# Performance work log

Measured on AMD Instinct MI355X. Metric: run time of the kernel, lower is better.

Reference implementation:

```python
import jax, jax.numpy as jnp
import numpy as np

H = 8      # num_attention_heads
DH = 96    # attention_head_size
LN_EPS = 1e-5


def setup_inputs() -> dict:
    key = jax.random.key(0)
    ks = jax.random.split(key, 12)
    B, S, D = 2, 768, 768
    sc = 0.02
    return {
        "hidden_states": jax.random.normal(ks[0], (B, S, D), jnp.float32),
        "distance_matrix": jax.random.uniform(ks[1], (B, S, S), jnp.float32) * 20.0,
        "angle_matrix": jax.random.uniform(ks[2], (B, S, S), jnp.float32) * np.pi,
        "attention_mask": jnp.ones((B, S), jnp.float32),
        "Wq": jax.random.normal(ks[3], (D, D), jnp.float32) * sc,
        "bq": jnp.zeros((D,), jnp.float32),
        "Wk": jax.random.normal(ks[4], (D, D), jnp.float32) * sc,
        "bk": jnp.zeros((D,), jnp.float32),
        "Wv": jax.random.normal(ks[5], (D, D), jnp.float32) * sc,
        "bv": jnp.zeros((D,), jnp.float32),
        "Wd": jax.random.normal(ks[6], (DH,), jnp.float32) * sc,
        "bd": jnp.zeros((DH,), jnp.float32),
        "Wa": jax.random.normal(ks[7], (DH,), jnp.float32) * sc,
        "ba": jnp.zeros((DH,), jnp.float32),
        "Wo": jax.random.normal(ks[8], (D, D), jnp.float32) * sc,
        "bo": jnp.zeros((D,), jnp.float32),
        "ln_g": jnp.ones((D,), jnp.float32),
        "ln_b": jnp.zeros((D,), jnp.float32),
    }


def _heads(x, B, S):
    # [B,S,D] -> [B,H,S,DH]
    return x.reshape(B, S, H, DH).transpose(0, 2, 1, 3)


def reference(hidden_states, distance_matrix, angle_matrix, attention_mask,
              Wq, bq, Wk, bk, Wv, bv, Wd, bd, Wa, ba, Wo, bo, ln_g, ln_b):
    B, S, D = hidden_states.shape
    q = _heads(hidden_states @ Wq.T + bq, B, S)   # [B,H,S,DH]
    k = _heads(hidden_states @ Wk.T + bk, B, S)
    v = _heads(hidden_states @ Wv.T + bv, B, S)

    scores = jnp.einsum('bhid,bhjd->bhij', q, k) / jnp.sqrt(jnp.float32(DH))

    # distance / angle relative-position biases: emb[b,i,j,:] = dist[b,i,j]*Wd + bd
    dist_emb = distance_matrix[..., None] * Wd + bd   # [B,S,S,DH]
    scores = scores + jnp.einsum('bhid,bijd->bhij', q, dist_emb)
    ang_emb = angle_matrix[..., None] * Wa + ba       # [B,S,S,DH]
    scores = scores + jnp.einsum('bhid,bijd->bhij', q, ang_emb)

    # key mask, broadcast over heads and query positions
    scores = scores + (1.0 - attention_mask)[:, None, None, :] * -10000.0

    probs = jax.nn.softmax(scores, axis=-1)           # [B,H,S,S]
    ctx = jnp.einsum('bhij,bhjd->bhid', probs, v)
    ctx = ctx.transpose(0, 2, 1, 3).reshape(B, S, D)  # [B,S,D]

    out = ctx @ Wo.T + bo
    x = out + hidden_states
    mu = jnp.mean(x, axis=-1, keepdims=True)
    var = jnp.var(x, axis=-1, keepdims=True)
    out = (x - mu) * jax.lax.rsqrt(var + LN_EPS) * ln_g + ln_b
    return out, probs
```

## Files before the change

### kernel.cpp

```cpp
#include <hip/hip_runtime.h>
#include <stdint.h>

#define B_  2
#define S_  768
#define D_  768
#define H_  8
#define DH_ 96

typedef unsigned short ushort_t;
typedef __bf16 bf16x8 __attribute__((ext_vector_type(8)));
typedef float  f32x4  __attribute__((ext_vector_type(4)));

__device__ inline ushort_t f2bf(float f) {
    union { float f; unsigned int u; } v; v.f = f;
    unsigned int u = v.u;
    unsigned int r = u + 0x7fffu + ((u >> 16) & 1u);
    return (ushort_t)(r >> 16);
}
__device__ inline float bf2f(ushort_t u) {
    union { unsigned int i; float f; } c; c.i = ((unsigned int)u) << 16;
    return c.f;
}

__device__ inline void glds16(const void* gp, void* lp) {
    auto g = reinterpret_cast<const __attribute__((address_space(1))) uint32_t*>(
        reinterpret_cast<uintptr_t>(gp));
    auto l = reinterpret_cast<__attribute__((address_space(3))) uint32_t*>(
        reinterpret_cast<uintptr_t>(lp));
    __builtin_amdgcn_global_load_lds(g, l, 16, 0, 0);
}

__global__ __launch_bounds__(256) void k_convert(
        const float* __restrict__ X, const float* __restrict__ Wq,
        const float* __restrict__ Wk, const float* __restrict__ Wv,
        const float* __restrict__ Wo,
        ushort_t* __restrict__ Xb, ushort_t* __restrict__ Wb) {
    const int NX4 = (B_ * S_ * D_) / 4;
    const int NW4 = (D_ * D_) / 4;
    int i = blockIdx.x * blockDim.x + threadIdx.x;
    float4 v;
    ushort_t* dst;
    if (i < NX4) {
        v = ((const float4*)X)[i];
        dst = Xb + i * 4;
    } else {
        int wi = i - NX4;
        int sel = wi / NW4;
        int off = wi - sel * NW4;
        const float* src = (sel == 0) ? Wq : (sel == 1) ? Wk : (sel == 2) ? Wv : Wo;
        v = ((const float4*)src)[off];
        dst = Wb + wi * 4;
    }
    ushort4 o;
    o.x = f2bf(v.x); o.y = f2bf(v.y); o.z = f2bf(v.z); o.w = f2bf(v.w);
    *(ushort4*)dst = o;
}

__device__ inline void gemm64_dbuf(
        const ushort_t* __restrict__ A, int lda,
        const ushort_t* __restrict__ Bt, int ldb,
        int K, int m0, int n0,
        ushort_t* As, ushort_t* Bs, f32x4 acc[2][2]) {
    const int tid  = threadIdx.x;
    const int lane = tid & 63, wave = tid >> 6;
    const int wm = (wave >> 1) * 32, wn = (wave & 1) * 32;
    const int fr = lane & 15, fk = (lane >> 4) * 8;
    const ushort_t* Ap = A  + (size_t)(m0 + wave * 16 + (lane >> 2)) * lda + (lane & 3) * 8;
    const ushort_t* Bp = Bt + (size_t)(n0 + wave * 16 + (lane >> 2)) * ldb + (lane & 3) * 8;
    glds16(Ap, As + wave * 512);
    glds16(Bp, Bs + wave * 512);
    for (int kt = 0; kt < K; kt += 32) {
        const int cur = (kt >> 5) & 1;
        __syncthreads();
        if (kt + 32 < K) {
            glds16(Ap + kt + 32, As + (cur ^ 1) * 2048 + wave * 512);
            glds16(Bp + kt + 32, Bs + (cur ^ 1) * 2048 + wave * 512);
        }
        const ushort_t* Ab = As + cur * 2048;
        const ushort_t* Bb = Bs + cur * 2048;
        bf16x8 a0 = *(const bf16x8*)&Ab[(wm      + fr) * 32 + fk];
        bf16x8 a1 = *(const bf16x8*)&Ab[(wm + 16 + fr) * 32 + fk];
        bf16x8 b0 = *(const bf16x8*)&Bb[(wn      + fr) * 32 + fk];
        bf16x8 b1 = *(const bf16x8*)&Bb[(wn + 16 + fr) * 32 + fk];
        acc[0][0] = __builtin_amdgcn_mfma_f32_16x16x32_bf16(a0, b0, acc[0][0], 0, 0, 0);
        acc[0][1] = __builtin_amdgcn_mfma_f32_16x16x32_bf16(a0, b1, acc[0][1], 0, 0, 0);
        acc[1][0] = __builtin_amdgcn_mfma_f32_16x16x32_bf16(a1, b0, acc[1][0], 0, 0, 0);
        acc[1][1] = __builtin_amdgcn_mfma_f32_16x16x32_bf16(a1, b1, acc[1][1], 0, 0, 0);
    }
}

__global__ __launch_bounds__(256) void k_qkv(
        const ushort_t* __restrict__ Xb, const ushort_t* __restrict__ Wb,
        const float* __restrict__ bq, const float* __restrict__ bk,
        const float* __restrict__ bv,
        ushort_t* __restrict__ Qb, ushort_t* __restrict__ Kb,
        ushort_t* __restrict__ Vtb) {
    __shared__ __align__(16) ushort_t As[2 * 64 * 32];
    __shared__ __align__(16) ushort_t Bs[2 * 64 * 32];
    f32x4 acc[2][2];
    #pragma unroll
    for (int i = 0; i < 2; i++)
        #pragma unroll
        for (int j = 0; j < 2; j++) acc[i][j] = (f32x4){0.f, 0.f, 0.f, 0.f};
    const int m0 = blockIdx.y * 64, n0 = blockIdx.x * 64;
    gemm64_dbuf(Xb, D_, Wb, D_, D_, m0, n0, As, Bs, acc);
    const int lane = threadIdx.x & 63, wave = threadIdx.x >> 6;
    const int wm = (wave >> 1) * 32, wn = (wave & 1) * 32;
    #pragma unroll
    for (int ni = 0; ni < 2; ni++) {
        int gcol = n0 + wn + ni * 16 + (lane & 15);
        int gsel = gcol / D_, d768 = gcol - gsel * D_;
        int h = d768 / DH_, d = d768 - h * DH_;
        float bias = (gsel == 0 ? bq : (gsel == 1 ? bk : bv))[d768];
        #pragma unroll
        for (int mi = 0; mi < 2; mi++) {
            int grow0 = m0 + wm + mi * 16 + (lane >> 4) * 4;
            int b = grow0 / S_, s0 = grow0 - b * S_;
            int bh = b * H_ + h;
            if (gsel == 2) {
                ushort4 o4;
                o4.x = f2bf(acc[mi][ni][0] + bias);
                o4.y = f2bf(acc[mi][ni][1] + bias);
                o4.z = f2bf(acc[mi][ni][2] + bias);
                o4.w = f2bf(acc[mi][ni][3] + bias);
                *(ushort4*)&Vtb[((size_t)bh * DH_ + d) * S_ + s0] = o4;
            } else {
                #pragma unroll
                for (int r = 0; r < 4; r++) {
                    ushort_t ob = f2bf(acc[mi][ni][r] + bias);
                    if (gsel == 0) Qb[((size_t)bh * S_ + s0 + r) * DH_ + d] = ob;
                    else           Kb[((size_t)bh * S_ + s0 + r) * DH_ + d] = ob;
                }
            }
        }
    }
}

__global__ __launch_bounds__(256) void k_qcoef(
        const ushort_t* __restrict__ Qb,
        const float* __restrict__ Wd, const float* __restrict__ bd,
        const float* __restrict__ Wa, const float* __restrict__ ba,
        float* __restrict__ qcoef) {
    const int wave = threadIdx.x >> 6, lane = threadIdx.x & 63;
    const int row = blockIdx.x * 4 + wave;
    const ushort_t* q = Qb + (size_t)row * DH_;
    float e0 = bf2f(q[lane]);
    float c0 = e0 * Wd[lane];
    float c1 = e0 * Wa[lane];
    float c2 = e0 * (bd[lane] + ba[lane]);
    if (lane < 32) {
        int d = 64 + lane;
        float e1 = bf2f(q[d]);
        c0 += e1 * Wd[d];
        c1 += e1 * Wa[d];
        c2 += e1 * (bd[d] + ba[d]);
    }
    #pragma unroll
    for (int o = 32; o > 0; o >>= 1) {
        c0 += __shfl_down(c0, o);
        c1 += __shfl_down(c1, o);
        c2 += __shfl_down(c2, o);
    }
    if (lane == 0) {
        qcoef[row * 3 + 0] = c0;
        qcoef[row * 3 + 1] = c1;
        qcoef[row * 3 + 2] = c2;
    }
}

#define FL1B 20480
__global__ __launch_bounds__(256, 3) void k_flash(
        const ushort_t* __restrict__ Qb, const ushort_t* __restrict__ Kb,
        const ushort_t* __restrict__ Vtb, const float* __restrict__ qcoef,
        const float* __restrict__ distm, const float* __restrict__ angm,
        const float* __restrict__ mask,
        float* __restrict__ probs, ushort_t* __restrict__ Ctxb) {
    __shared__ __align__(16) char sm[2 * FL1B + 512];
    float* mstat = (float*)(sm + 2 * FL1B);
    float* lstat = (float*)(sm + 2 * FL1B + 256);
    const int idx = blockIdx.x;
    const int h = idx / 96, rem = idx - h * 96;
    const int b = rem / 48, r0 = (rem - b * 48) * 16;
    const int bh = b * H_ + h;
    const int tid = threadIdx.x, lane = tid & 63, w = tid >> 6;
    const int frn = lane & 15, g = lane >> 4;
    const ushort_t* Qbh = Qb + (size_t)bh * S_ * DH_;
    const ushort_t* Kbh = Kb + (size_t)bh * S_ * DH_;
    const ushort_t* Vbh = Vtb + (size_t)bh * DH_ * S_;

    auto stage = [&](int c) {
        char* bufc = sm + (c & 1) * FL1B;
        ushort_t* Ks = (ushort_t*)bufc;
        const ushort_t* kg = Kbh + (size_t)c * 64 * DH_;
        #pragma unroll
        for (int t = 0; t < 3; ++t) {
            int grp = w * 3 + t;
            glds16(kg + (size_t)lane * DH_ + grp * 8, Ks + grp * 512);
        }
        int row = 4 * w + g;
        int colb = (frn ^ (row & 7)) << 2;
        size_t src = ((size_t)b * S_ + r0 + row) * S_ + c * 64 + colb;
        glds16(distm + src, (float*)(bufc + 12288) + w * 256);
        glds16(angm  + src, (float*)(bufc + 16384) + w * 256);
    };

    stage(0);

    bf16x8 aq0, aq1, aq2;
    {
        const ushort_t* qp = Qbh + (size_t)(r0 + frn) * DH_ + g * 8;
        aq0 = *(const bf16x8*)qp;
        aq1 = *(const bf16x8*)(qp + 32);
        aq2 = *(const bf16x8*)(qp + 64);
    }
    float qc0, qc1, qc2;
    {
        const float* qp = qcoef + ((size_t)bh * S_ + r0 + frn) * 3;
        qc0 = qp[0]; qc1 = qp[1]; qc2 = qp[2];
    }
    const float isq = 0.10206207261596577f;
    const int dswz = ((4 * w + g) ^ (frn & 7)) << 2;
    const int jrow = (16 * w + frn) * 8;

    f32x4 acc[12];
    __syncthreads();
    #pragma unroll
    for (int c = 0; c < 12; ++c) {
        if (c < 11) stage(c + 1);
        char* bufc = sm + (c & 1) * FL1B;
        const ushort_t* Ks = (const ushort_t*)bufc;
        const float* Dd = (const float*)(bufc + 12288);
        const float* Da = (const float*)(bufc + 16384);
        bf16x8 k0 = *(const bf16x8*)&Ks[(g    ) * 512 + jrow];
        bf16x8 k1 = *(const bf16x8*)&Ks[(g + 4) * 512 + jrow];
        bf16x8 k2 = *(const bf16x8*)&Ks[(g + 8) * 512 + jrow];
        f32x4 ca = (f32x4){0.f, 0.f, 0.f, 0.f};
        ca = __builtin_amdgcn_mfma_f32_16x16x32_bf16(k0, aq0, ca, 0, 0, 0);
        ca = __builtin_amdgcn_mfma_f32_16x16x32_bf16(k1, aq1, ca, 0, 0, 0);
        ca = __builtin_amdgcn_mfma_f32_16x16x32_bf16(k2, aq2, ca, 0, 0, 0);
        float4 d4 = *(const float4*)(Dd + frn * 64 + dswz);
        float4 a4 = *(const float4*)(Da + frn * 64 + dswz);
        float4 m4 = *(const float4*)(mask + b * S_ + c * 64 + w * 16 + g * 4);
        f32x4 o;
        o[0] = ca[0] * isq + d4.x * qc0 + a4.x * qc1 + qc2 + (1.f - m4.x) * -10000.f;
        o[1] = ca[1] * isq + d4.y * qc0 + a4.y * qc1 + qc2 + (1.f - m4.y) * -10000.f;
        o[2] = ca[2] * isq + d4.z * qc0 + a4.z * qc1 + qc2 + (1.f - m4.z) * -10000.f;
        o[3] = ca[3] * isq + d4.w * qc0 + a4.w * qc1 + qc2 + (1.f - m4.w) * -10000.f;
        acc[c] = o;
        __syncthreads();
    }

    float mx = -1e30f;
    #pragma unroll
    for (int c = 0; c < 12; ++c)
        #pragma unroll
        for (int r = 0; r < 4; ++r) mx = fmaxf(mx, acc[c][r]);
    mx = fmaxf(mx, __shfl_xor(mx, 16));
    mx = fmaxf(mx, __shfl_xor(mx, 32));
    if (g == 0) mstat[w * 16 + frn] = mx;
    __syncthreads();
    float mf = fmaxf(fmaxf(mstat[frn], mstat[16 + frn]),
                     fmaxf(mstat[32 + frn], mstat[48 + frn]));
    float sum = 0.f;
    #pragma unroll
    for (int c = 0; c < 12; ++c)
        #pragma unroll
        for (int r = 0; r < 4; ++r) {
            float e = __expf(acc[c][r] - mf);
            acc[c][r] = e;
            sum += e;
        }
    sum += __shfl_xor(sum, 16);
    sum += __shfl_xor(sum, 32);
    if (g == 0) lstat[w * 16 + frn] = sum;
    __syncthreads();
    float inv = 1.f / (lstat[frn] + lstat[16 + frn] + lstat[32 + frn] + lstat[48 + frn]);

    float* ctxred = (float*)sm;
    {
        int zr = tid >> 4, zc = tid & 15;
        #pragma unroll
        for (int i = 0; i < 6; ++i) ctxred[zr * 100 + i * 16 + zc] = 0.f;
    }
    __syncthreads();

    f32x4 accO[6];
    #pragma unroll
    for (int i = 0; i < 6; ++i) accO[i] = (f32x4){0.f, 0.f, 0.f, 0.f};
    float* prow = probs + ((size_t)bh * S_ + r0 + frn) * S_ + w * 16 + g * 4;
    const ushort_t* vbase = Vbh + (size_t)frn * S_ + w * 16 + g * 4;
    #pragma unroll
    for (int c = 0; c < 12; c += 2) {
        float4 p;
        p.x = acc[c][0] * inv; p.y = acc[c][1] * inv;
        p.z = acc[c][2] * inv; p.w = acc[c][3] * inv;
        *(float4*)(prow + c * 64) = p;
        p.x = acc[c + 1][0] * inv; p.y = acc[c + 1][1] * inv;
        p.z = acc[c + 1][2] * inv; p.w = acc[c + 1][3] * inv;
        *(float4*)(prow + (c + 1) * 64) = p;
        union { bf16x8 v; ushort_t u[8]; } pa;
        #pragma unroll
        for (int r = 0; r < 4; ++r) {
            pa.u[r]     = f2bf(acc[c][r]);
            pa.u[r + 4] = f2bf(acc[c + 1][r]);
        }
        #pragma unroll
        for (int nt = 0; nt < 6; ++nt) {
            const ushort_t* vp = vbase + (size_t)nt * 16 * S_ + c * 64;
            union { bf16x8 v; uint2 q2[2]; } vb;
            vb.q2[0] = *(const uint2*)vp;
            vb.q2[1] = *(const uint2*)(vp + 64);
            accO[nt] = __builtin_amdgcn_mfma_f32_16x16x32_bf16(pa.v, vb.v, accO[nt], 0, 0, 0);
        }
    }
    #pragma unroll
    for (int nt = 0; nt < 6; ++nt)
        #pragma unroll
        for (int r = 0; r < 4; ++r)
            atomicAdd(&ctxred[(4 * g + r) * 100 + nt * 16 + frn], accO[nt][r]);
    __syncthreads();
    {
        int zr = tid >> 4, zc = tid & 15;
        float ivr = 1.f / (lstat[zr] + lstat[16 + zr] + lstat[32 + zr] + lstat[48 + zr]);
        ushort_t* crow = Ctxb + ((size_t)b * S_ + r0 + zr) * D_ + h * DH_;
        #pragma unroll
        for (int i = 0; i < 6; ++i)
            crow[i * 16 + zc] = f2bf(ctxred[zr * 100 + i * 16 + zc] * ivr);
    }
}

__global__ __launch_bounds__(256) void k_out(
        const ushort_t* __restrict__ Ctxb, const ushort_t* __restrict__ Wob,
        const float* __restrict__ bo, const float* __restrict__ hidden,
        float* __restrict__ xbuf) {
    __shared__ __align__(16) ushort_t As[2 * 64 * 32];
    __shared__ __align__(16) ushort_t Bs[2 * 64 * 32];
    f32x4 acc[2][2];
    #pragma unroll
    for (int i = 0; i < 2; i++)
        #pragma unroll
        for (int j = 0; j < 2; j++) acc[i][j] = (f32x4){0.f, 0.f, 0.f, 0.f};
    const int m0 = blockIdx.y * 64, n0 = blockIdx.x * 64;
    gemm64_dbuf(Ctxb, D_, Wob, D_, D_, m0, n0, As, Bs, acc);
    const int lane = threadIdx.x & 63, wave = threadIdx.x >> 6;
    const int wm = (wave >> 1) * 32, wn = (wave & 1) * 32;
    #pragma unroll
    for (int ni = 0; ni < 2; ni++) {
        int gcol = n0 + wn + ni * 16 + (lane & 15);
        float bias = bo[gcol];
        #pragma unroll
        for (int mi = 0; mi < 2; mi++) {
            #pragma unroll
            for (int r = 0; r < 4; r++) {
                int grow = m0 + wm + mi * 16 + (lane >> 4) * 4 + r;
                xbuf[(size_t)grow * D_ + gcol] =
                    acc[mi][ni][r] + bias + hidden[(size_t)grow * D_ + gcol];
            }
        }
    }
}

__global__ __launch_bounds__(256) void k_ln(
        const float* __restrict__ xbuf, const float* __restrict__ g,
        const float* __restrict__ bb, float* __restrict__ out) {
    const float* x = xbuf + (size_t)blockIdx.x * D_;
    const int t = threadIdx.x;
    float a0 = x[t], a1 = x[t + 256], a2 = x[t + 512];
    float s = a0 + a1 + a2;
    float ss = a0 * a0 + a1 * a1 + a2 * a2;
    __shared__ float r1[4], r2[4];
    #pragma unroll
    for (int o = 32; o > 0; o >>= 1) { s += __shfl_down(s, o); ss += __shfl_down(ss, o); }
    if ((t & 63) == 0) { r1[t >> 6] = s; r2[t >> 6] = ss; }
    __syncthreads();
    float ts = r1[0] + r1[1] + r1[2] + r1[3];
    float tss = r2[0] + r2[1] + r2[2] + r2[3];
    float mu = ts * (1.0f / D_);
    float var = tss * (1.0f / D_) - mu * mu;
    float rstd = rsqrtf(var + 1e-5f);
    float* o = out + (size_t)blockIdx.x * D_;
    o[t]       = (a0 - mu) * rstd * g[t]       + bb[t];
    o[t + 256] = (a1 - mu) * rstd * g[t + 256] + bb[t + 256];
    o[t + 512] = (a2 - mu) * rstd * g[t + 512] + bb[t + 512];
}

extern "C" void kernel_launch(void* const* d_in, const int* in_sizes, int n_in,
                              void* d_out, int out_size, void* d_ws, size_t ws_size,
                              hipStream_t stream) {
    const float* X     = (const float*)d_in[0];
    const float* distm = (const float*)d_in[1];
    const float* angm  = (const float*)d_in[2];
    const float* mask  = (const float*)d_in[3];
    const float* Wq    = (const float*)d_in[4];
    const float* bq    = (const float*)d_in[5];
    const float* Wk    = (const float*)d_in[6];
    const float* bk    = (const float*)d_in[7];
    const float* Wv    = (const float*)d_in[8];
    const float* bv    = (const float*)d_in[9];
    const float* Wd    = (const float*)d_in[10];
    const float* bd    = (const float*)d_in[11];
    const float* Wa    = (const float*)d_in[12];
    const float* ba    = (const float*)d_in[13];
    const float* Wo    = (const float*)d_in[14];
    const float* bo    = (const float*)d_in[15];
    const float* ln_g  = (const float*)d_in[16];
    const float* ln_b  = (const float*)d_in[17];

    float* outp  = (float*)d_out;
    float* probs = (float*)d_out + (size_t)B_ * S_ * D_;

    char* ws = (char*)d_ws;
    ushort_t* Xb    = (ushort_t*)(ws + 0);
    ushort_t* Wb    = (ushort_t*)(ws + 2359296);
    ushort_t* Qb    = (ushort_t*)(ws + 7077888);
    ushort_t* Kb    = (ushort_t*)(ws + 9437184);
    ushort_t* Vtb   = (ushort_t*)(ws + 11796480);
    ushort_t* Ctxb  = (ushort_t*)(ws + 14155776);
    float*    qcoef = (float*)   (ws + 16515072);
    float*    xbuf  = (float*)   (ws + 16662528);

    k_convert<<<3456, 256, 0, stream>>>(X, Wq, Wk, Wv, Wo, Xb, Wb);
    k_qkv<<<dim3(36, 24), 256, 0, stream>>>(Xb, Wb, bq, bk, bv, Qb, Kb, Vtb);
    k_qcoef<<<3072, 256, 0, stream>>>(Qb, Wd, bd, Wa, ba, qcoef);
    k_flash<<<768, 256, 0, stream>>>(Qb, Kb, Vtb, qcoef, distm, angm, mask, probs, Ctxb);
    k_out<<<dim3(12, 24), 256, 0, stream>>>(Ctxb, Wb + (size_t)2304 * 768, bo, X, xbuf);
    k_ln<<<1536, 256, 0, stream>>>(xbuf, ln_g, ln_b, outp);
}
```

Measured before the change: 207.6 us.

## Stage V through double-buffered LDS and store K in chunked-d layout

K is now written by the QKV projection in a [bh][d/8][S][8] layout, so each 16-byte async global-to-LDS load in the flash kernel reads a contiguous span instead of striding by the head dimension. The PV phase no longer reads V directly from global memory with 8-byte loads. It async-copies 128-column V tiles into a double-buffered, XOR-swizzled LDS region, overlapping the next tile's load with the current MFMAs. This raises shared memory per block (2x24KB plus stats) and adds barriers per tile, which could reduce occupancy under the 3-blocks launch bound.

```diff
diff --git a/kernel.cpp b/kernel.cpp
--- a/kernel.cpp
+++ b/kernel.cpp
@@ -124,12 +124,17 @@
                 o4.z = f2bf(acc[mi][ni][2] + bias);
                 o4.w = f2bf(acc[mi][ni][3] + bias);
                 *(ushort4*)&Vtb[((size_t)bh * DH_ + d) * S_ + s0] = o4;
+            } else if (gsel == 1) {
+                #pragma unroll
+                for (int r = 0; r < 4; r++) {
+                    ushort_t ob = f2bf(acc[mi][ni][r] + bias);
+                    Kb[(((size_t)bh * 12 + (d >> 3)) * S_ + s0 + r) * 8 + (d & 7)] = ob;
+                }
             } else {
                 #pragma unroll
                 for (int r = 0; r < 4; r++) {
                     ushort_t ob = f2bf(acc[mi][ni][r] + bias);
-                    if (gsel == 0) Qb[((size_t)bh * S_ + s0 + r) * DH_ + d] = ob;
-                    else           Kb[((size_t)bh * S_ + s0 + r) * DH_ + d] = ob;
+                    Qb[((size_t)bh * S_ + s0 + r) * DH_ + d] = ob;
                 }
             }
         }
@@ -169,15 +174,16 @@
 }
 
 #define FL1B 20480
+#define VBUF 24576
 __global__ __launch_bounds__(256, 3) void k_flash(
         const ushort_t* __restrict__ Qb, const ushort_t* __restrict__ Kb,
         const ushort_t* __restrict__ Vtb, const float* __restrict__ qcoef,
         const float* __restrict__ distm, const float* __restrict__ angm,
         const float* __restrict__ mask,
         float* __restrict__ probs, ushort_t* __restrict__ Ctxb) {
-    __shared__ __align__(16) char sm[2 * FL1B + 512];
-    float* mstat = (float*)(sm + 2 * FL1B);
-    float* lstat = (float*)(sm + 2 * FL1B + 256);
+    __shared__ __align__(16) char sm[2 * VBUF + 512];
+    float* mstat = (float*)(sm + 2 * VBUF);
+    float* lstat = (float*)(sm + 2 * VBUF + 256);
     const int idx = blockIdx.x;
     const int h = idx / 96, rem = idx - h * 96;
     const int b = rem / 48, r0 = (rem - b * 48) * 16;
@@ -185,23 +191,33 @@
     const int tid = threadIdx.x, lane = tid & 63, w = tid >> 6;
     const int frn = lane & 15, g = lane >> 4;
     const ushort_t* Qbh = Qb + (size_t)bh * S_ * DH_;
-    const ushort_t* Kbh = Kb + (size_t)bh * S_ * DH_;
+    const ushort_t* Kbh = Kb + (size_t)bh * 12 * S_ * 8;
     const ushort_t* Vbh = Vtb + (size_t)bh * DH_ * S_;
 
     auto stage = [&](int c) {
         char* bufc = sm + (c & 1) * FL1B;
         ushort_t* Ks = (ushort_t*)bufc;
-        const ushort_t* kg = Kbh + (size_t)c * 64 * DH_;
         #pragma unroll
         for (int t = 0; t < 3; ++t) {
             int grp = w * 3 + t;
-            glds16(kg + (size_t)lane * DH_ + grp * 8, Ks + grp * 512);
+            glds16(Kbh + (((size_t)grp * S_ + c * 64 + lane) << 3), Ks + grp * 512);
         }
         int row = 4 * w + g;
         int colb = (frn ^ (row & 7)) << 2;
         size_t src = ((size_t)b * S_ + r0 + row) * S_ + c * 64 + colb;
         glds16(distm + src, (float*)(bufc + 12288) + w * 256);
         glds16(angm  + src, (float*)(bufc + 16384) + w * 256);
+    };
+    auto stage_v = [&](int p) {
+        ushort_t* Vs = (ushort_t*)(sm + (p & 1) * VBUF);
+        const int c0 = p * 128;
+        #pragma unroll
+        for (int t = 0; t < 6; ++t) {
+            int q = w * 6 + t;
+            int d = 4 * q + (lane >> 4);
+            int ug = (lane & 15) ^ (d & 15);
+            glds16(Vbh + (size_t)d * S_ + c0 + ug * 8, Vs + q * 512);
+        }
     };
 
     stage(0);
@@ -250,6 +266,7 @@
         __syncthreads();
     }
 
+    stage_v(0);
     float mx = -1e30f;
     #pragma unroll
     for (int c = 0; c < 12; ++c)
@@ -276,6 +293,42 @@
     __syncthreads();
     float inv = 1.f / (lstat[frn] + lstat[16 + frn] + lstat[32 + frn] + lstat[48 + frn]);
 
+    f32x4 accO[6];
+    #pragma unroll
+    for (int i = 0; i < 6; ++i) accO[i] = (f32x4){0.f, 0.f, 0.f, 0.f};
+    float* prow = probs + ((size_t)bh * S_ + r0 + frn) * S_ + w * 16 + g * 4;
+    const int vsub = (g & 1) << 2;
+    const int u0 = 2 * w + (g >> 1);
+    #pragma unroll
+    for (int p = 0; p < 6; ++p) {
+        if (p < 5) stage_v(p + 1);
+        const ushort_t* Vs = (const ushort_t*)(sm + (p & 1) * VBUF);
+        const int c = 2 * p;
+        float4 pw;
+        pw.x = acc[c][0] * inv; pw.y = acc[c][1] * inv;
+        pw.z = acc[c][2] * inv; pw.w = acc[c][3] * inv;
+        *(float4*)(prow + c * 64) = pw;
+        pw.x = acc[c + 1][0] * inv; pw.y = acc[c + 1][1] * inv;
+        pw.z = acc[c + 1][2] * inv; pw.w = acc[c + 1][3] * inv;
+        *(float4*)(prow + (c + 1) * 64) = pw;
+        union { bf16x8 v; ushort_t u[8]; } pa;
+        #pragma unroll
+        for (int r = 0; r < 4; ++r) {
+            pa.u[r]     = f2bf(acc[c][r]);
+            pa.u[r + 4] = f2bf(acc[c + 1][r]);
+        }
+        #pragma unroll
+        for (int nt = 0; nt < 6; ++nt) {
+            int d = nt * 16 + frn;
+            const ushort_t* vr = Vs + d * 128 + vsub;
+            union { bf16x8 v; uint2 q2[2]; } vb;
+            vb.q2[0] = *(const uint2*)(vr + (((u0    ) ^ frn) << 3));
+            vb.q2[1] = *(const uint2*)(vr + (((u0 + 8) ^ frn) << 3));
+            accO[nt] = __builtin_amdgcn_mfma_f32_16x16x32_bf16(pa.v, vb.v, accO[nt], 0, 0, 0);
+        }
+        __syncthreads();
+    }
+
     float* ctxred = (float*)sm;
     {
         int zr = tid >> 4, zc = tid & 15;
@@ -283,36 +336,6 @@
         for (int i = 0; i < 6; ++i) ctxred[zr * 100 + i * 16 + zc] = 0.f;
     }
     __syncthreads();
-
-    f32x4 accO[6];
-    #pragma unroll
-    for (int i = 0; i < 6; ++i) accO[i] = (f32x4){0.f, 0.f, 0.f, 0.f};
-    float* prow = probs + ((size_t)bh * S_ + r0 + frn) * S_ + w * 16 + g * 4;
-    const ushort_t* vbase = Vbh + (size_t)frn * S_ + w * 16 + g * 4;
-    #pragma unroll
-    for (int c = 0; c < 12; c += 2) {
-        float4 p;
-        p.x = acc[c][0] * inv; p.y = acc[c][1] * inv;
-        p.z = acc[c][2] * inv; p.w = acc[c][3] * inv;
-        *(float4*)(prow + c * 64) = p;
-        p.x = acc[c + 1][0] * inv; p.y = acc[c + 1][1] * inv;
-        p.z = acc[c + 1][2] * inv; p.w = acc[c + 1][3] * inv;
-        *(float4*)(prow + (c + 1) * 64) = p;
-        union { bf16x8 v; ushort_t u[8]; } pa;
-        #pragma unroll
-        for (int r = 0; r < 4; ++r) {
-            pa.u[r]     = f2bf(acc[c][r]);
-            pa.u[r + 4] = f2bf(acc[c + 1][r]);
-        }
-        #pragma unroll
-        for (int nt = 0; nt < 6; ++nt) {
-            const ushort_t* vp = vbase + (size_t)nt * 16 * S_ + c * 64;
-            union { bf16x8 v; uint2 q2[2]; } vb;
-            vb.q2[0] = *(const uint2*)vp;
-            vb.q2[1] = *(const uint2*)(vp + 64);
-            accO[nt] = __builtin_amdgcn_mfma_f32_16x16x32_bf16(pa.v, vb.v, accO[nt], 0, 0, 0);
-        }
-    }
     #pragma unroll
     for (int nt = 0; nt < 6; ++nt)
         #pragma unroll
```

After: 190.6 us. 1.09x faster.
